# Kernel tuning notes

Measured on AMD Instinct MI355X. Metric: run time of the kernel, lower is better.

The kernel has to match this reference:

```python
import jax, jax.numpy as jnp
import numpy as np

B, S, D_IN, D_OUT = 4, 2048, 4096, 4096


def setup_inputs() -> dict:
    key = jax.random.key(0)
    k1, k2, k3 = jax.random.split(key, 3)
    # int32 activations (already quantized upstream in the original pipeline)
    x_i32 = jax.random.randint(k1, (B, S, D_IN), -128, 128, dtype=jnp.int32)
    # int8 weights in [in, out] layout (Linear weight transposed), symmetric range [-127, 127]
    weight_i8 = jax.random.randint(k2, (D_IN, D_OUT), -127, 128, dtype=jnp.int32).astype(jnp.int8)
    # bias quantized affine to int32 (scale=16 in original)
    bias_i32 = jax.random.randint(k3, (D_OUT,), -2048, 2048, dtype=jnp.int32)
    return {"x_i32": x_i32, "weight_i8": weight_i8, "bias_i32": bias_i32, "out_shift": 7}


def reference(x_i32, weight_i8, bias_i32, out_shift):
    x_shape = x_i32.shape
    x2d = x_i32.reshape(-1, x_shape[-1]).astype(jnp.int32)  # [tokens, d_in]
    # int8 weights upcast to int32, plain int32 matmul with int32 accumulation
    y = jnp.matmul(x2d, weight_i8.astype(jnp.int32), preferred_element_type=jnp.int32)
    y = y + bias_i32  # fused bias add (int32)
    if out_shift > 0:  # out_shift is a static Python int
        y = jnp.right_shift(y, out_shift)  # arithmetic shift on signed int32
    return y.reshape(*x_shape[:-1], y.shape[-1]).astype(jnp.int32)
```

## Files before the change

kernel.cpp:

```cpp
#include <hip/hip_runtime.h>

using int32x4 = __attribute__((ext_vector_type(4))) int;

#define BM 256
#define BN 256
#define BKB 128
#define HT 16384
#define BUF 65536

__global__ __launch_bounds__(256) void pack_x_kernel(const int32x4* __restrict__ x,
                                                     int32x4* __restrict__ xp,
                                                     int nvec) {
    int t = blockIdx.x * 256 + threadIdx.x;
    if (t >= nvec) return;
    int32x4 a = x[t * 4 + 0];
    int32x4 b = x[t * 4 + 1];
    int32x4 c = x[t * 4 + 2];
    int32x4 d = x[t * 4 + 3];
    int32x4 o;
    o.x = (a.x & 255) | ((a.y & 255) << 8) | ((a.z & 255) << 16) | (a.w << 24);
    o.y = (b.x & 255) | ((b.y & 255) << 8) | ((b.z & 255) << 16) | (b.w << 24);
    o.z = (c.x & 255) | ((c.y & 255) << 8) | ((c.z & 255) << 16) | (c.w << 24);
    o.w = (d.x & 255) | ((d.y & 255) << 8) | ((d.z & 255) << 16) | (d.w << 24);
    xp[t] = o;
}

__global__ __launch_bounds__(256) void transform_w_kernel(const int* __restrict__ w,
                                                          unsigned char* __restrict__ wt,
                                                          int K, int N) {
    __shared__ unsigned char tileT[64][72];
    int tx = threadIdx.x & 15;
    int ty = threadIdx.x >> 4;
    int n0 = blockIdx.x * 64;
    int k0 = blockIdx.y * 64;
#pragma unroll
    for (int r = 0; r < 4; ++r) {
        int row = ty * 4 + r;
        int32x4 v = *(const int32x4*)&w[(size_t)(k0 + row) * N + n0 + tx * 4];
        tileT[tx * 4 + 0][row] = (unsigned char)(v.x & 255);
        tileT[tx * 4 + 1][row] = (unsigned char)(v.y & 255);
        tileT[tx * 4 + 2][row] = (unsigned char)(v.z & 255);
        tileT[tx * 4 + 3][row] = (unsigned char)(v.w & 255);
    }
    __syncthreads();
#pragma unroll
    for (int r = 0; r < 4; ++r) {
        int row = ty * 4 + r;
        uchar4 v = *(const uchar4*)&tileT[row][tx * 4];
        *(uchar4*)&wt[(size_t)(n0 + row) * K + k0 + tx * 4] = v;
    }
}

__global__ __launch_bounds__(512, 2) void gemm_i8_8ph(
    const char* __restrict__ A,
    const char* __restrict__ Bt,
    const int* __restrict__ bias,
    const int* __restrict__ shiftp,
    int* __restrict__ C,
    int M, int N, int K) {
    __shared__ char smem[2 * BUF];

    const int nbn = N / BN;
    const int nwg = gridDim.x;
    const int bid = blockIdx.x;
    const int cpx = nwg >> 3;
    const int swz = (bid & 7) * cpx + (bid >> 3);
    const int m0 = (swz / nbn) * BM;
    const int n0 = (swz % nbn) * BN;

    const int t = threadIdx.x;
    const int lane = t & 63;
    const int wave = t >> 6;
    const int wr = wave >> 2;
    const int wc = wave & 3;

    const int s_row = t >> 2;
    const int s_col = ((t & 3) << 4) ^ (((t >> 3) & 3) << 4);
    const char* a_src = A + (size_t)(m0 + s_row) * K + s_col;
    const char* b_src = Bt + (size_t)(n0 + s_row) * K + s_col;
    const size_t jstr = (size_t)128 * K;
    char* lds_st = smem + t * 16;

    const int lr = lane & 15;
    const int lc = (lane >> 4) << 4;
    const int xr = ((lr >> 1) & 3) << 4;
    const int a_off = ((wr << 7) + lr) * 64 + (lc ^ xr);
    const int b_off = HT + ((wc << 6) + lr) * 64 + (lc ^ xr);

    int32x4 acc[8][4] = {};

    const int nt = K / BKB;

#define GLL(src, dst)                                                 \
    __builtin_amdgcn_global_load_lds(                                 \
        (const __attribute__((address_space(1))) void*)(src),        \
        (__attribute__((address_space(3))) void*)(dst), 16, 0, 0)

#define STAGE(mat, kcol, h, b)                                   \
    do {                                                         \
        GLL((mat) + (kcol), lds_st + (b)*BUF + (h)*HT);          \
        GLL((mat) + jstr + (kcol), lds_st + (b)*BUF + (h)*HT + 8192); \
    } while (0)

#define FENCE asm volatile("" ::: "memory")
#define BARR                           \
    do {                               \
        FENCE;                         \
        __builtin_amdgcn_s_barrier();  \
        FENCE;                         \
    } while (0)
#define LGKM0                                                   \
    do {                                                        \
        asm volatile("s_waitcnt lgkmcnt(0)" ::: "memory");      \
        __builtin_amdgcn_sched_barrier(0);                      \
    } while (0)
#define VMW(n)                                                  \
    do {                                                        \
        asm volatile("s_waitcnt vmcnt(" #n ")" ::: "memory");   \
        __builtin_amdgcn_sched_barrier(0);                      \
    } while (0)

    STAGE(a_src, 0, 0, 0);
    STAGE(b_src, 0, 1, 0);
    STAGE(a_src, 64, 2, 0);
    STAGE(b_src, 64, 3, 0);
    VMW(4);
    BARR;

    for (int tt = 0; tt < nt; ++tt) {
        const int cur = tt & 1;
        const int nxt = cur ^ 1;
        const size_t kc = (size_t)(tt + 1) * BKB;
        const bool st = (tt + 1) < nt;
        const int ab = cur * BUF + a_off;
        const int bb = cur * BUF + b_off;
        int32x4 af[4], bf[4];

#pragma unroll
        for (int i = 0; i < 4; ++i) af[i] = *(const int32x4*)&smem[ab + i * 1024];
#pragma unroll
        for (int i = 0; i < 4; ++i) bf[i] = *(const int32x4*)&smem[bb + i * 1024];
        if (st) STAGE(a_src, kc, 0, nxt);
        BARR;
        LGKM0;
        __builtin_amdgcn_s_setprio(1);
#pragma unroll
        for (int i = 0; i < 4; ++i)
#pragma unroll
            for (int j = 0; j < 4; ++j)
                acc[i][j] = __builtin_amdgcn_mfma_i32_16x16x64_i8(af[i], bf[j], acc[i][j], 0, 0, 0);
        __builtin_amdgcn_s_setprio(0);
        BARR;

#pragma unroll
        for (int i = 0; i < 4; ++i) af[i] = *(const int32x4*)&smem[ab + (4 + i) * 1024];
        if (st) STAGE(b_src, kc, 1, nxt);
        BARR;
        LGKM0;
        __builtin_amdgcn_s_setprio(1);
#pragma unroll
        for (int i = 0; i < 4; ++i)
#pragma unroll
            for (int j = 0; j < 4; ++j)
                acc[4 + i][j] = __builtin_amdgcn_mfma_i32_16x16x64_i8(af[i], bf[j], acc[4 + i][j], 0, 0, 0);
        __builtin_amdgcn_s_setprio(0);
        if (st) { VMW(4); } else { VMW(0); }
        BARR;

#pragma unroll
        for (int i = 0; i < 4; ++i) af[i] = *(const int32x4*)&smem[ab + 32768 + i * 1024];
#pragma unroll
        for (int i = 0; i < 4; ++i) bf[i] = *(const int32x4*)&smem[bb + 32768 + i * 1024];
        if (st) STAGE(a_src, kc + 64, 2, nxt);
        BARR;
        LGKM0;
        __builtin_amdgcn_s_setprio(1);
#pragma unroll
        for (int i = 0; i < 4; ++i)
#pragma unroll
            for (int j = 0; j < 4; ++j)
                acc[i][j] = __builtin_amdgcn_mfma_i32_16x16x64_i8(af[i], bf[j], acc[i][j], 0, 0, 0);
        __builtin_amdgcn_s_setprio(0);
        BARR;

#pragma unroll
        for (int i = 0; i < 4; ++i) af[i] = *(const int32x4*)&smem[ab + 32768 + (4 + i) * 1024];
        if (st) STAGE(b_src, kc + 64, 3, nxt);
        BARR;
        LGKM0;
        __builtin_amdgcn_s_setprio(1);
#pragma unroll
        for (int i = 0; i < 4; ++i)
#pragma unroll
            for (int j = 0; j < 4; ++j)
                acc[4 + i][j] = __builtin_amdgcn_mfma_i32_16x16x64_i8(af[i], bf[j], acc[4 + i][j], 0, 0, 0);
        __builtin_amdgcn_s_setprio(0);
        if (st) VMW(4);
        BARR;
    }

    const int s = *shiftp;
    const int crow = (lane >> 4) << 2;
    const int ccol = lane & 15;
    int bv[4];
#pragma unroll
    for (int nf = 0; nf < 4; ++nf) bv[nf] = bias[n0 + wc * 64 + nf * 16 + ccol];
#pragma unroll
    for (int mf = 0; mf < 8; ++mf) {
        const int grow0 = m0 + wr * 128 + mf * 16 + crow;
#pragma unroll
        for (int nf = 0; nf < 4; ++nf) {
            const int gcol = n0 + wc * 64 + nf * 16 + ccol;
#pragma unroll
            for (int r = 0; r < 4; ++r) {
                int y = acc[mf][nf][r] + bv[nf];
                y = (s > 0) ? (y >> s) : y;
                C[(size_t)(grow0 + r) * N + gcol] = y;
            }
        }
    }
#undef GLL
#undef STAGE
#undef FENCE
#undef BARR
#undef LGKM0
#undef VMW
}

extern "C" void kernel_launch(void* const* d_in, const int* in_sizes, int n_in,
                              void* d_out, int out_size, void* d_ws, size_t ws_size,
                              hipStream_t stream) {
    const int* x = (const int*)d_in[0];
    const int* w = (const int*)d_in[1];
    const int* bias = (const int*)d_in[2];
    const int* shiftp = (const int*)d_in[3];
    int* out = (int*)d_out;

    const int N = in_sizes[2];
    const int K = in_sizes[1] / N;
    const int M = in_sizes[0] / K;

    char* xp = (char*)d_ws;
    unsigned char* wt = (unsigned char*)d_ws + (size_t)M * K;

    int nvec = (int)(((long long)M * K) / 16);
    pack_x_kernel<<<(nvec + 255) / 256, 256, 0, stream>>>((const int32x4*)x, (int32x4*)xp, nvec);

    dim3 tgrid(N / 64, K / 64);
    transform_w_kernel<<<tgrid, 256, 0, stream>>>(w, wt, K, N);

    int nwg = (M / BM) * (N / BN);
    gemm_i8_8ph<<<nwg, 512, 0, stream>>>(xp, (const char*)wt, bias, shiftp, out, M, N, K);
}
```

Baseline: 193.5 us.

## Replace double-buffered K=128 pipeline with 4-stage ring of K=64 LDS tiles

Restructures the GEMM main loop from two 64KB buffers, each holding a K=128 tile, into a four-slot ring of 32KB K=64 tiles with three tiles prefetched ahead. Total LDS stays at 128KB. Each tile keeps the two-phase A/B split MFMA schedule, and the vmcnt waits are reworked so three tiles of loads are in flight. The goal is deeper prefetch to hide global-to-LDS latency better. The cost is more barriers per K unit, plus a drain epilogue that is unrolled through a macro.

```diff
diff --git a/kernel.cpp b/kernel.cpp
--- a/kernel.cpp
+++ b/kernel.cpp
@@ -4,9 +4,7 @@
 
 #define BM 256
 #define BN 256
-#define BKB 128
-#define HT 16384
-#define BUF 65536
+#define TBUF 32768
 
 __global__ __launch_bounds__(256) void pack_x_kernel(const int32x4* __restrict__ x,
                                                      int32x4* __restrict__ xp,
@@ -51,14 +49,14 @@
     }
 }
 
-__global__ __launch_bounds__(512, 2) void gemm_i8_8ph(
+__global__ __launch_bounds__(512, 2) void gemm_i8_deep(
     const char* __restrict__ A,
     const char* __restrict__ Bt,
     const int* __restrict__ bias,
     const int* __restrict__ shiftp,
     int* __restrict__ C,
     int M, int N, int K) {
-    __shared__ char smem[2 * BUF];
+    __shared__ char smem[4 * TBUF];
 
     const int nbn = N / BN;
     const int nwg = gridDim.x;
@@ -85,22 +83,16 @@
     const int lc = (lane >> 4) << 4;
     const int xr = ((lr >> 1) & 3) << 4;
     const int a_off = ((wr << 7) + lr) * 64 + (lc ^ xr);
-    const int b_off = HT + ((wc << 6) + lr) * 64 + (lc ^ xr);
+    const int b_off = 16384 + ((wc << 6) + lr) * 64 + (lc ^ xr);
 
     int32x4 acc[8][4] = {};
 
-    const int nt = K / BKB;
+    const int nt = K / 64;
 
 #define GLL(src, dst)                                                 \
     __builtin_amdgcn_global_load_lds(                                 \
         (const __attribute__((address_space(1))) void*)(src),        \
         (__attribute__((address_space(3))) void*)(dst), 16, 0, 0)
-
-#define STAGE(mat, kcol, h, b)                                   \
-    do {                                                         \
-        GLL((mat) + (kcol), lds_st + (b)*BUF + (h)*HT);          \
-        GLL((mat) + jstr + (kcol), lds_st + (b)*BUF + (h)*HT + 8192); \
-    } while (0)
 
 #define FENCE asm volatile("" ::: "memory")
 #define BARR                           \
@@ -120,84 +112,62 @@
         __builtin_amdgcn_sched_barrier(0);                      \
     } while (0)
 
-    STAGE(a_src, 0, 0, 0);
-    STAGE(b_src, 0, 1, 0);
-    STAGE(a_src, 64, 2, 0);
-    STAGE(b_src, 64, 3, 0);
-    VMW(4);
+#define TILE(TT, DOSTAGE, VMWSTMT)                                                     \
+    do {                                                                               \
+        const int base_ = ((TT) & 3) * TBUF;                                           \
+        const int sb_ = (((TT) + 3) & 3) * TBUF;                                       \
+        const size_t kc_ = (size_t)((TT) + 3) * 64;                                    \
+        int32x4 af[4], bf[4];                                                          \
+        _Pragma("unroll") for (int i = 0; i < 4; ++i)                                  \
+            af[i] = *(const int32x4*)&smem[base_ + a_off + i * 1024];                  \
+        _Pragma("unroll") for (int i = 0; i < 4; ++i)                                  \
+            bf[i] = *(const int32x4*)&smem[base_ + b_off + i * 1024];                  \
+        if (DOSTAGE) {                                                                 \
+            GLL(a_src + kc_, lds_st + sb_);                                            \
+            GLL(a_src + jstr + kc_, lds_st + sb_ + 8192);                              \
+        }                                                                              \
+        BARR;                                                                          \
+        LGKM0;                                                                         \
+        __builtin_amdgcn_s_setprio(1);                                                 \
+        _Pragma("unroll") for (int i = 0; i < 4; ++i)                                  \
+            _Pragma("unroll") for (int j = 0; j < 4; ++j)                              \
+                acc[i][j] =                                                            \
+                    __builtin_amdgcn_mfma_i32_16x16x64_i8(af[i], bf[j], acc[i][j], 0, 0, 0); \
+        __builtin_amdgcn_s_setprio(0);                                                 \
+        BARR;                                                                          \
+        _Pragma("unroll") for (int i = 0; i < 4; ++i)                                  \
+            af[i] = *(const int32x4*)&smem[base_ + a_off + (4 + i) * 1024];            \
+        if (DOSTAGE) {                                                                 \
+            GLL(b_src + kc_, lds_st + sb_ + 16384);                                    \
+            GLL(b_src + jstr + kc_, lds_st + sb_ + 16384 + 8192);                      \
+        }                                                                              \
+        BARR;                                                                          \
+        LGKM0;                                                                         \
+        __builtin_amdgcn_s_setprio(1);                                                 \
+        _Pragma("unroll") for (int i = 0; i < 4; ++i)                                  \
+            _Pragma("unroll") for (int j = 0; j < 4; ++j)                              \
+                acc[4 + i][j] =                                                        \
+                    __builtin_amdgcn_mfma_i32_16x16x64_i8(af[i], bf[j], acc[4 + i][j], 0, 0, 0); \
+        __builtin_amdgcn_s_setprio(0);                                                 \
+        VMWSTMT;                                                                       \
+        BARR;                                                                          \
+    } while (0)
+
+#pragma unroll
+    for (int p = 0; p < 3; ++p) {
+        GLL(a_src + p * 64, lds_st + p * TBUF);
+        GLL(a_src + jstr + p * 64, lds_st + p * TBUF + 8192);
+        GLL(b_src + p * 64, lds_st + p * TBUF + 16384);
+        GLL(b_src + jstr + p * 64, lds_st + p * TBUF + 24576);
+    }
+    VMW(8);
     BARR;
 
-    for (int tt = 0; tt < nt; ++tt) {
-        const int cur = tt & 1;
-        const int nxt = cur ^ 1;
-        const size_t kc = (size_t)(tt + 1) * BKB;
-        const bool st = (tt + 1) < nt;
-        const int ab = cur * BUF + a_off;
-        const int bb = cur * BUF + b_off;
-        int32x4 af[4], bf[4];
-
-#pragma unroll
-        for (int i = 0; i < 4; ++i) af[i] = *(const int32x4*)&smem[ab + i * 1024];
-#pragma unroll
-        for (int i = 0; i < 4; ++i) bf[i] = *(const int32x4*)&smem[bb + i * 1024];
-        if (st) STAGE(a_src, kc, 0, nxt);
-        BARR;
-        LGKM0;
-        __builtin_amdgcn_s_setprio(1);
-#pragma unroll
-        for (int i = 0; i < 4; ++i)
-#pragma unroll
-            for (int j = 0; j < 4; ++j)
-                acc[i][j] = __builtin_amdgcn_mfma_i32_16x16x64_i8(af[i], bf[j], acc[i][j], 0, 0, 0);
-        __builtin_amdgcn_s_setprio(0);
-        BARR;
-
-#pragma unroll
-        for (int i = 0; i < 4; ++i) af[i] = *(const int32x4*)&smem[ab + (4 + i) * 1024];
-        if (st) STAGE(b_src, kc, 1, nxt);
-        BARR;
-        LGKM0;
-        __builtin_amdgcn_s_setprio(1);
-#pragma unroll
-        for (int i = 0; i < 4; ++i)
-#pragma unroll
-            for (int j = 0; j < 4; ++j)
-                acc[4 + i][j] = __builtin_amdgcn_mfma_i32_16x16x64_i8(af[i], bf[j], acc[4 + i][j], 0, 0, 0);
-        __builtin_amdgcn_s_setprio(0);
-        if (st) { VMW(4); } else { VMW(0); }
-        BARR;
-
-#pragma unroll
-        for (int i = 0; i < 4; ++i) af[i] = *(const int32x4*)&smem[ab + 32768 + i * 1024];
-#pragma unroll
-        for (int i = 0; i < 4; ++i) bf[i] = *(const int32x4*)&smem[bb + 32768 + i * 1024];
-        if (st) STAGE(a_src, kc + 64, 2, nxt);
-        BARR;
-        LGKM0;
-        __builtin_amdgcn_s_setprio(1);
-#pragma unroll
-        for (int i = 0; i < 4; ++i)
-#pragma unroll
-            for (int j = 0; j < 4; ++j)
-                acc[i][j] = __builtin_amdgcn_mfma_i32_16x16x64_i8(af[i], bf[j], acc[i][j], 0, 0, 0);
-        __builtin_amdgcn_s_setprio(0);
-        BARR;
-
-#pragma unroll
-        for (int i = 0; i < 4; ++i) af[i] = *(const int32x4*)&smem[ab + 32768 + (4 + i) * 1024];
-        if (st) STAGE(b_src, kc + 64, 3, nxt);
-        BARR;
-        LGKM0;
-        __builtin_amdgcn_s_setprio(1);
-#pragma unroll
-        for (int i = 0; i < 4; ++i)
-#pragma unroll
-            for (int j = 0; j < 4; ++j)
-                acc[4 + i][j] = __builtin_amdgcn_mfma_i32_16x16x64_i8(af[i], bf[j], acc[4 + i][j], 0, 0, 0);
-        __builtin_amdgcn_s_setprio(0);
-        if (st) VMW(4);
-        BARR;
-    }
+    int tt = 0;
+    for (; tt < nt - 3; ++tt) TILE(tt, 1, VMW(8));
+    TILE(tt, 0, VMW(4)); ++tt;
+    TILE(tt, 0, VMW(0)); ++tt;
+    TILE(tt, 0, (void)0);
 
     const int s = *shiftp;
     const int crow = (lane >> 4) << 2;
@@ -220,11 +190,11 @@
         }
     }
 #undef GLL
-#undef STAGE
 #undef FENCE
 #undef BARR
 #undef LGKM0
 #undef VMW
+#undef TILE
 }
 
 extern "C" void kernel_launch(void* const* d_in, const int* in_sizes, int n_in,
@@ -250,5 +220,5 @@
     transform_w_kernel<<<tgrid, 256, 0, stream>>>(w, wt, K, N);
 
     int nwg = (M / BM) * (N / BN);
-    gemm_i8_8ph<<<nwg, 512, 0, stream>>>(xp, (const char*)wt, bias, shiftp, out, M, N, K);
-}
+    gemm_i8_deep<<<nwg, 512, 0, stream>>>(xp, (const char*)wt, bias, shiftp, out, M, N, K);
+}
```

New measurement: 188.8 us. 1.03x faster.
